# Performance work log

Measured on AMD Instinct MI355X. Metric: run time of the kernel, lower is better.

## Reference

```python
import jax, jax.numpy as jnp
from jax import lax
import numpy as np

NPOINTS, GROUP_SIZE, RADIUS = 1024, 32, 0.2
MLP = [64, 64, 128]
IN_CH = 6
BN_EPS = 1e-5


def farthest_point_sample(xyz, npoints):
    # xyz: [B, N, 3] -> idx [B, npoints]
    B, N, _ = xyz.shape

    def step(carry, _):
        dists, farthest = carry                      # [B,N], [B]
        centroid = jnp.take_along_axis(xyz, farthest[:, None, None], axis=1)  # [B,1,3]
        d = jnp.sum((xyz - centroid) ** 2, axis=-1)  # [B,N]
        dists = jnp.minimum(dists, d)
        nxt = jnp.argmax(dists, axis=-1).astype(jnp.int32)
        return (dists, nxt), farthest

    init = (jnp.full((B, N), 1e10, dtype=xyz.dtype), jnp.zeros((B,), dtype=jnp.int32))
    _, idxs = lax.scan(step, init, None, length=npoints)
    return idxs.T  # [B, npoints]


def ball_query(new_xyz, xyz, r, gs):
    # new_xyz: [B,S,3], xyz: [B,N,3] -> idx [B,S,gs]
    B, N, _ = xyz.shape
    sq = jnp.sum((new_xyz[:, :, None, :] - xyz[:, None, :, :]) ** 2, axis=-1)  # [B,S,N]
    idx = jnp.where(sq <= r * r, jnp.arange(N, dtype=jnp.int32), N)
    idx = jnp.sort(idx, axis=-1)[..., :gs]          # first gs in-ball indices
    first = idx[..., :1]
    idx = jnp.where(idx == N, first, idx)           # pad with first neighbor
    return idx


_batched_gather = jax.vmap(lambda p, i: p[i])        # p:[N,C], i:[S,G] -> [S,G,C]


def sample_and_group(xyz, features, npoints, gs, r):
    fps_idx = farthest_point_sample(xyz, npoints)                 # [B,S]
    new_xyz = jnp.take_along_axis(xyz, fps_idx[..., None], axis=1)  # [B,S,3]
    idx = ball_query(new_xyz, xyz, r, gs)                         # [B,S,G]
    grouped_xyz = _batched_gather(xyz, idx) - new_xyz[:, :, None, :]  # [B,S,G,3]
    grouped_feat = _batched_gather(features, idx)                 # [B,S,G,C]
    group_features = jnp.concatenate([grouped_xyz, grouped_feat], axis=-1)  # [B,S,G,3+C]
    return new_xyz, group_features


def pointnet(group_features, ws, bs, gammas, betas):
    # group_features: [B,S,G,D] -> permute to [B,D,S,G]
    x = jnp.transpose(group_features, (0, 3, 1, 2))
    for w, b, g, beta in zip(ws, bs, gammas, betas):
        x = jnp.einsum('oc,bcsg->bosg', w, x) + b[None, :, None, None]
        mu = jnp.mean(x, axis=(0, 2, 3), keepdims=True)
        var = jnp.mean((x - mu) ** 2, axis=(0, 2, 3), keepdims=True)  # biased, train-mode BN
        x = (x - mu) * lax.rsqrt(var + BN_EPS)
        x = x * g[None, :, None, None] + beta[None, :, None, None]
        x = jax.nn.relu(x)
    x = jnp.max(x, axis=-1)                         # max over group dim -> [B,C,S]
    return jnp.transpose(x, (0, 2, 1))              # [B,S,C]


def setup_inputs() -> dict:
    key = jax.random.key(0)
    ks = jax.random.split(key, 16)
    xyz = jax.random.uniform(ks[0], (16, 8192, 3), dtype=jnp.float32)
    features = jax.random.normal(ks[1], (16, 8192, 3), dtype=jnp.float32)
    inp = {'xyz': xyz, 'features': features}
    in_ch = IN_CH
    for i, out_ch in enumerate(MLP):
        scale = 1.0 / np.sqrt(in_ch)
        inp[f'w{i}'] = jax.random.uniform(ks[2 + 4 * i], (out_ch, in_ch), jnp.float32, -scale, scale)
        inp[f'b{i}'] = jax.random.uniform(ks[3 + 4 * i], (out_ch,), jnp.float32, -scale, scale)
        inp[f'g{i}'] = jnp.ones((out_ch,), jnp.float32)
        inp[f'bt{i}'] = jnp.zeros((out_ch,), jnp.float32)
        in_ch = out_ch
    return inp


def reference(xyz, features, w0, b0, g0, bt0, w1, b1, g1, bt1, w2, b2, g2, bt2):
    new_xyz, group_features = sample_and_group(xyz, features, NPOINTS, GROUP_SIZE, RADIUS)
    abstract_features = pointnet(group_features, [w0, w1, w2], [b0, b1, b2],
                                 [g0, g1, g2], [bt0, bt1, bt2])
    return new_xyz, abstract_features
```

## Files before the change

### kernel.cpp

```cpp
#include <hip/hip_runtime.h>
#include <math.h>

#define BB 16
#define NN 8192
#define SS 1024
#define GG 32
#define MTOT (BB*SS*GG)

struct alignas(16) f4 { float v[4]; };

typedef __attribute__((ext_vector_type(8))) short bfrag;
typedef __attribute__((ext_vector_type(4))) float facc;

#define MFMA16(a, b, c) __builtin_amdgcn_mfma_f32_16x16x32_bf16(a, b, c, 0, 0, 0)

__device__ __forceinline__ unsigned short f2bf(float f) {
    const unsigned u = __float_as_uint(f);
    return (unsigned short)((u + 0x7FFFu + ((u >> 16) & 1u)) >> 16);
}
__device__ __forceinline__ unsigned packbf(float lo, float hi) {
    return (unsigned)f2bf(lo) | ((unsigned)f2bf(hi) << 16);
}

template<int CTRL>
__device__ __forceinline__ int dppmov(int x) {
    return __builtin_amdgcn_update_dpp(x, x, CTRL, 0xF, 0xF, true);
}
template<int CTRL>
__device__ __forceinline__ void dlevel(int& hi, int& lo) {
    const int oh = dppmov<CTRL>(hi);
    const int ol = dppmov<CTRL>(lo);
    const unsigned long long o =
        ((unsigned long long)(unsigned)oh << 32) | (unsigned)ol;
    const unsigned long long c =
        ((unsigned long long)(unsigned)hi << 32) | (unsigned)lo;
    if (o > c) { hi = oh; lo = ol; }
}

__global__ __launch_bounds__(256) void fps_kernel(const float* __restrict__ xyz,
                                                  float* __restrict__ newxyz)
{
    __shared__ float lx[NN], ly[NN], lz[NN];
    __shared__ unsigned long long slots[2][4];
    const int b = blockIdx.x;
    const int t = threadIdx.x;
    const int wave = t >> 6, lane = t & 63;
    const float* base = xyz + (size_t)b * NN * 3;

    float px[32], py[32], pz[32], dd[32];
#pragma unroll
    for (int k = 0; k < 32; ++k) {
        const int p = (k << 8) + t;
        const float x = base[p * 3 + 0];
        const float y = base[p * 3 + 1];
        const float z = base[p * 3 + 2];
        px[k] = x; py[k] = y; pz[k] = z; dd[k] = 1e10f;
        lx[p] = x; ly[p] = y; lz[p] = z;
    }
    __syncthreads();

    int far = 0;
    float* outb = newxyz + (size_t)b * SS * 3;
    for (int s = 0; s < SS; ++s) {
        const float cx = lx[far], cy = ly[far], cz = lz[far];
        if (t == 0) {
            outb[s * 3 + 0] = cx;
            outb[s * 3 + 1] = cy;
            outb[s * 3 + 2] = cz;
        }
        float bf = -1.f;
        unsigned binv = 0u;
#pragma unroll
        for (int k = 0; k < 32; ++k) {
            const float dx = __fsub_rn(px[k], cx);
            const float dy = __fsub_rn(py[k], cy);
            const float dz = __fsub_rn(pz[k], cz);
            const float d  = __fadd_rn(__fadd_rn(__fmul_rn(dx, dx), __fmul_rn(dy, dy)),
                                       __fmul_rn(dz, dz));
            const float nd = fminf(dd[k], d);
            dd[k] = nd;
            if (nd > bf) {
                bf = nd;
                binv = 0xFFFFFFFFu - (unsigned)((k << 8) + t);
            }
        }

        int hi = __float_as_int(bf);
        int lo = (int)binv;
        dlevel<0x121>(hi, lo);
        dlevel<0x122>(hi, lo);
        dlevel<0x124>(hi, lo);
        dlevel<0x128>(hi, lo);
        {
            const int oh = __shfl_xor(hi, 16), ol = __shfl_xor(lo, 16);
            const unsigned long long o =
                ((unsigned long long)(unsigned)oh << 32) | (unsigned)ol;
            const unsigned long long c =
                ((unsigned long long)(unsigned)hi << 32) | (unsigned)lo;
            if (o > c) { hi = oh; lo = ol; }
        }
        {
            const int oh = __shfl_xor(hi, 32), ol = __shfl_xor(lo, 32);
            const unsigned long long o =
                ((unsigned long long)(unsigned)oh << 32) | (unsigned)ol;
            const unsigned long long c =
                ((unsigned long long)(unsigned)hi << 32) | (unsigned)lo;
            if (o > c) { hi = oh; lo = ol; }
        }

        if (lane == 0)
            slots[s & 1][wave] =
                ((unsigned long long)(unsigned)hi << 32) | (unsigned)lo;
        __syncthreads();
        unsigned long long g = slots[s & 1][0];
#pragma unroll
        for (int w = 1; w < 4; ++w) {
            const unsigned long long o = slots[s & 1][w];
            g = (o > g) ? o : g;
        }
        far = (int)(0xFFFFFFFFu - (unsigned)(g & 0xFFFFFFFFull));
    }
}

__global__ __launch_bounds__(256) void ball_gather_kernel(const float* __restrict__ xyz,
                                                          const float* __restrict__ feat,
                                                          const float* __restrict__ newxyz,
                                                          float* __restrict__ v,
                                                          float* __restrict__ part1)
{
    const int wid  = (int)((blockIdx.x * 256 + threadIdx.x) >> 6);
    const int lane = threadIdx.x & 63;
    if (wid >= BB * SS) return;
    const int b = wid >> 10;

    const float cx = newxyz[wid * 3 + 0];
    const float cy = newxyz[wid * 3 + 1];
    const float cz = newxyz[wid * 3 + 2];
    const float* xb = xyz + (size_t)b * NN * 3;
    const float* fb = feat + (size_t)b * NN * 3;
    const size_t mbase = (size_t)wid * GG;

    float mS[6];
    float mP[36];
#pragma unroll
    for (int c = 0; c < 6; ++c) mS[c] = 0.f;
#pragma unroll
    for (int c = 0; c < 36; ++c) mP[c] = 0.f;

    int cnt = 0, firstp = -1;
    for (int base = 0; base < NN && cnt < GG; base += 64) {
        const int p = base + lane;
        const float x = xb[p * 3 + 0], y = xb[p * 3 + 1], z = xb[p * 3 + 2];
        const float dx = __fsub_rn(cx, x);
        const float dy = __fsub_rn(cy, y);
        const float dz = __fsub_rn(cz, z);
        const float d  = __fadd_rn(__fadd_rn(__fmul_rn(dx, dx), __fmul_rn(dy, dy)),
                                   __fmul_rn(dz, dz));
        const bool hit = (d <= 0.04f);
        const unsigned long long m = __ballot(hit);
        if (firstp < 0 && m != 0ull) firstp = base + (int)__builtin_ctzll(m);
        const int pos = cnt + (int)__popcll(m & ((1ull << lane) - 1ull));
        if (hit && pos < GG) {
            const size_t mm = mbase + pos;
            float a[6];
            a[0] = __fsub_rn(x, cx);
            a[1] = __fsub_rn(y, cy);
            a[2] = __fsub_rn(z, cz);
            a[3] = fb[p * 3 + 0];
            a[4] = fb[p * 3 + 1];
            a[5] = fb[p * 3 + 2];
#pragma unroll
            for (int c = 0; c < 6; ++c) {
                v[(size_t)c * MTOT + mm] = a[c];
                mS[c] += a[c];
#pragma unroll
                for (int dch = 0; dch < 6; ++dch)
                    mP[c * 6 + dch] = fmaf(a[c], a[dch], mP[c * 6 + dch]);
            }
        }
        cnt += (int)__popcll(m);
    }
    if (cnt < GG) {
        const int p = firstp;
        const float x = xb[p * 3 + 0], y = xb[p * 3 + 1], z = xb[p * 3 + 2];
        float a[6];
        a[0] = __fsub_rn(x, cx);
        a[1] = __fsub_rn(y, cy);
        a[2] = __fsub_rn(z, cz);
        a[3] = fb[p * 3 + 0];
        a[4] = fb[p * 3 + 1];
        a[5] = fb[p * 3 + 2];
        for (int j = cnt + lane; j < GG; j += 64) {
            const size_t mm = mbase + j;
#pragma unroll
            for (int c = 0; c < 6; ++c) {
                v[(size_t)c * MTOT + mm] = a[c];
                mS[c] += a[c];
#pragma unroll
                for (int dch = 0; dch < 6; ++dch)
                    mP[c * 6 + dch] = fmaf(a[c], a[dch], mP[c * 6 + dch]);
            }
        }
    }
#pragma unroll
    for (int off = 1; off < 64; off <<= 1) {
#pragma unroll
        for (int c = 0; c < 6; ++c) mS[c] += __shfl_xor(mS[c], off);
#pragma unroll
        for (int c = 0; c < 36; ++c) mP[c] += __shfl_xor(mP[c], off);
    }
    if (lane == 0) {
        float* row = part1 + (size_t)wid * 42;
#pragma unroll
        for (int c = 0; c < 6; ++c) row[c] = mS[c];
#pragma unroll
        for (int c = 0; c < 36; ++c) row[6 + c] = mP[c];
    }
}

__global__ __launch_bounds__(1024) void finalize1_kernel(const float* __restrict__ part1,
                                                         const float* __restrict__ w0,
                                                         const float* __restrict__ g0,
                                                         const float* __restrict__ bt0,
                                                         const float* __restrict__ w1g,
                                                         const float* __restrict__ w2g,
                                                         short* __restrict__ wf1,
                                                         float* __restrict__ c1,
                                                         short* __restrict__ wf2r,
                                                         short* __restrict__ wf3r)
{
    const int tid = threadIdx.x;
    if (tid < 512) {
        const int f = tid >> 6, l = tid & 63;
        const int o = (f >> 1) * 16 + (l & 15);
        const int kb = (f & 1) * 32 + (l >> 4) * 8;
#pragma unroll
        for (int j = 0; j < 8; ++j)
            wf2r[tid * 8 + j] = (short)f2bf(w1g[o * 64 + kb + j]);
    }
    {
        const int f = tid >> 6, l = tid & 63;
        const int o = (f >> 1) * 16 + (l & 15);
        const int kb = (f & 1) * 32 + (l >> 4) * 8;
#pragma unroll
        for (int j = 0; j < 8; ++j)
            wf3r[tid * 8 + j] = (short)f2bf(w2g[o * 64 + kb + j]);
    }

    __shared__ double red[1008];
    __shared__ double tot[42];
    __shared__ float Asf[64];
    if (tid < 1008) {
        const int j = tid % 42, r = tid / 42;
        double s = 0.0;
#pragma unroll 4
        for (int i = r; i < BB * SS; i += 24) s += (double)part1[(size_t)i * 42 + j];
        red[tid] = s;
    }
    __syncthreads();
    if (tid < 42) {
        double s = 0.0;
        for (int r = 0; r < 24; ++r) s += red[r * 42 + tid];
        tot[tid] = s / (double)MTOT;
    }
    __syncthreads();
    if (tid < 64) {
        double m1 = 0.0;
        for (int c = 0; c < 6; ++c) m1 += (double)w0[tid * 6 + c] * tot[c];
        double e2 = 0.0;
        for (int c = 0; c < 6; ++c)
            for (int d = 0; d < 6; ++d)
                e2 += (double)w0[tid * 6 + c] * (double)w0[tid * 6 + d] * tot[6 + c * 6 + d];
        double var = e2 - m1 * m1;
        if (var < 0.0) var = 0.0;
        const double A = (double)g0[tid] / sqrt(var + 1e-5);
        Asf[tid] = (float)A;
        c1[tid] = (float)((double)bt0[tid] - A * m1);
    }
    __syncthreads();
    if (tid < 256) {
        const int l = tid & 63;
        const int o = (tid >> 6) * 16 + (l & 15);
        const int h = l >> 4;
#pragma unroll
        for (int j = 0; j < 8; ++j) {
            const float val = (h == 0 && j < 6) ? Asf[o] * w0[o * 6 + j] : 0.f;
            wf1[tid * 8 + j] = (short)f2bf(val);
        }
    }
}

template<int PHASE>
__global__ __launch_bounds__(256, 2) void chain_kernel(
    const float* __restrict__ v,
    const short* __restrict__ wf1, const float* __restrict__ c1,
    const short* __restrict__ wf2, const float* __restrict__ c2,
    const short* __restrict__ wf3,
    float* __restrict__ part, float* __restrict__ gmax, int tpb)
{
    __shared__ alignas(16) unsigned Hu1[4][16][36];
    __shared__ alignas(16) unsigned Hu2[(PHASE == 3) ? 4 : 1][16][36];
    __shared__ alignas(16) short w3l[(PHASE == 3) ? 8192 : 8];
    __shared__ alignas(16) float gm[(PHASE == 3) ? 4 : 1][128][20];
    __shared__ float redf[4][4][64];

    const int tid = threadIdx.x;
    const int w = tid >> 6, l = tid & 63;
    const int mcol = l & 15, h = l >> 4;

    if constexpr (PHASE == 3) {
        const unsigned* src = (const unsigned*)wf3;
        unsigned* dst = (unsigned*)w3l;
        for (int i = tid; i < 4096; i += 256) dst[i] = src[i];
    }
    __syncthreads();

    bfrag a1[4];
#pragma unroll
    for (int t = 0; t < 4; ++t) a1[t] = *(const bfrag*)&wf1[(t * 64 + l) * 8];
    bfrag a2[8];
#pragma unroll
    for (int f = 0; f < 8; ++f) a2[f] = *(const bfrag*)&wf2[(f * 64 + l) * 8];
    float c1v[16];
#pragma unroll
    for (int t = 0; t < 4; ++t)
#pragma unroll
        for (int r = 0; r < 4; ++r) c1v[t * 4 + r] = c1[t * 16 + h * 4 + r];
    float c2v[16];
    if constexpr (PHASE == 3) {
#pragma unroll
        for (int t = 0; t < 4; ++t)
#pragma unroll
            for (int r = 0; r < 4; ++r) c2v[t * 4 + r] = c2[t * 16 + h * 4 + r];
    }

    constexpr int NS = (PHASE == 3) ? 32 : 16;
    float sA[NS], qA[NS];
#pragma unroll
    for (int i = 0; i < NS; ++i) { sA[i] = 0.f; qA[i] = 0.f; }

    const facc zf = {0.f, 0.f, 0.f, 0.f};

    for (int ti = 0; ti < tpb; ++ti) {
        const int tile = blockIdx.x * tpb + ti;
        float mx[(PHASE == 3) ? 32 : 1];
        if constexpr (PHASE == 3) {
#pragma unroll
            for (int i = 0; i < 32; ++i) mx[i] = -3.0e38f;
        }

#pragma unroll
        for (int st = 0; st < 2; ++st) {
            const int mg = tile * 128 + w * 32 + st * 16 + mcol;

            bfrag bv;
#pragma unroll
            for (int j = 0; j < 8; ++j) bv[j] = 0;
            if (h == 0) {
#pragma unroll
                for (int j = 0; j < 6; ++j)
                    bv[j] = (short)f2bf(v[(size_t)j * MTOT + mg]);
            }
            facc x1[4];
#pragma unroll
            for (int t = 0; t < 4; ++t) x1[t] = MFMA16(a1[t], bv, zf);
#pragma unroll
            for (int t = 0; t < 4; ++t)
#pragma unroll
                for (int rr = 0; rr < 2; ++rr)
                    Hu1[w][mcol][t * 8 + h * 2 + rr] = packbf(
                        fmaxf(x1[t][2 * rr]     + c1v[t * 4 + 2 * rr],     0.f),
                        fmaxf(x1[t][2 * rr + 1] + c1v[t * 4 + 2 * rr + 1], 0.f));

            const bfrag b0 = *(const bfrag*)&Hu1[w][mcol][h * 4];
            const bfrag b1 = *(const bfrag*)&Hu1[w][mcol][16 + h * 4];

            if constexpr (PHASE == 2) {
#pragma unroll
                for (int t = 0; t < 4; ++t) {
                    facc a = MFMA16(a2[2 * t], b0, zf);
                    a = MFMA16(a2[2 * t + 1], b1, a);
#pragma unroll
                    for (int r = 0; r < 4; ++r) {
                        const float x = a[r];
                        sA[t * 4 + r] += x;
                        qA[t * 4 + r] = fmaf(x, x, qA[t * 4 + r]);
                    }
                }
            } else {
#pragma unroll
                for (int t = 0; t < 4; ++t) {
                    facc a = MFMA16(a2[2 * t], b0, zf);
                    a = MFMA16(a2[2 * t + 1], b1, a);
#pragma unroll
                    for (int rr = 0; rr < 2; ++rr)
                        Hu2[w][mcol][t * 8 + h * 2 + rr] = packbf(
                            fmaxf(a[2 * rr]     + c2v[t * 4 + 2 * rr],     0.f),
                            fmaxf(a[2 * rr + 1] + c2v[t * 4 + 2 * rr + 1], 0.f));
                }
                const bfrag d0 = *(const bfrag*)&Hu2[w][mcol][h * 4];
                const bfrag d1 = *(const bfrag*)&Hu2[w][mcol][16 + h * 4];
#pragma unroll
                for (int t3 = 0; t3 < 8; ++t3) {
                    const bfrag wa = *(const bfrag*)&w3l[((t3 * 2 + 0) * 64 + l) * 8];
                    const bfrag wb = *(const bfrag*)&w3l[((t3 * 2 + 1) * 64 + l) * 8];
                    facc a = MFMA16(wa, d0, zf);
                    a = MFMA16(wb, d1, a);
#pragma unroll
                    for (int r = 0; r < 4; ++r) {
                        const float x = a[r];
                        const int i = t3 * 4 + r;
                        sA[i] += x;
                        qA[i] = fmaf(x, x, qA[i]);
                        mx[i] = fmaxf(mx[i], x);
                    }
                }
            }
        }

        if constexpr (PHASE == 3) {
#pragma unroll
            for (int t3 = 0; t3 < 8; ++t3)
#pragma unroll
                for (int r = 0; r < 4; ++r)
                    gm[w][t3 * 16 + h * 4 + r][mcol] = mx[t3 * 4 + r];
            float m0 = -3.0e38f, m1 = -3.0e38f;
#pragma unroll
            for (int c4i = 0; c4i < 4; ++c4i) {
                const facc v0 = *(const facc*)&gm[w][2 * l][c4i * 4];
                const facc v1 = *(const facc*)&gm[w][2 * l + 1][c4i * 4];
#pragma unroll
                for (int jj = 0; jj < 4; ++jj) {
                    m0 = fmaxf(m0, v0[jj]);
                    m1 = fmaxf(m1, v1[jj]);
                }
            }
            const int g = tile * 4 + w;
            gmax[(size_t)g * 128 + 2 * l]     = m0;
            gmax[(size_t)g * 128 + 2 * l + 1] = m1;
        }
    }

#pragma unroll
    for (int off = 1; off < 16; off <<= 1) {
#pragma unroll
        for (int i = 0; i < NS; ++i) {
            sA[i] += __shfl_xor(sA[i], off);
            qA[i] += __shfl_xor(qA[i], off);
        }
    }
    __syncthreads();
    if (mcol == 0) {
#pragma unroll
        for (int i = 0; i < NS; ++i) {
            redf[w][h][i] = sA[i];
            redf[w][h][NS + i] = qA[i];
        }
    }
    __syncthreads();
    if constexpr (PHASE == 2) {
        if (tid < 128) {
            const int o = tid & 63, sq = tid >> 6;
            const int i = (o >> 4) * 4 + (o & 3), hh = (o >> 2) & 3;
            const int idx = sq * 16 + i;
            const float s = redf[0][hh][idx] + redf[1][hh][idx] +
                            redf[2][hh][idx] + redf[3][hh][idx];
            part[(size_t)blockIdx.x * 128 + sq * 64 + o] = s;
        }
    } else {
        if (tid < 256) {
            const int o = tid & 127, sq = tid >> 7;
            const int i = (o >> 4) * 4 + (o & 3), hh = (o >> 2) & 3;
            const int idx = sq * 32 + i;
            const float s = redf[0][hh][idx] + redf[1][hh][idx] +
                            redf[2][hh][idx] + redf[3][hh][idx];
            part[(size_t)blockIdx.x * 256 + sq * 128 + o] = s;
        }
    }
}

__global__ __launch_bounds__(1024) void finalize2_kernel(const float* __restrict__ part,
                                                         const float* __restrict__ w1g,
                                                         const float* __restrict__ g1,
                                                         const float* __restrict__ bt1,
                                                         short* __restrict__ wf2f,
                                                         float* __restrict__ c2)
{
    __shared__ double tot[1024];
    __shared__ float As[64];
    const int tid = threadIdx.x;
    const int j = tid & 127, r = tid >> 7;
    double s = 0.0;
#pragma unroll 4
    for (int blk = r; blk < 2048; blk += 8) s += (double)part[(size_t)blk * 128 + j];
    tot[tid] = s;
    __syncthreads();
    if (tid < 128) {
        double t = 0.0;
#pragma unroll
        for (int g = 0; g < 8; ++g) t += tot[g * 128 + tid];
        tot[tid] = t;
    }
    __syncthreads();
    if (tid < 64) {
        const double mean = tot[tid] / (double)MTOT;
        double var = tot[64 + tid] / (double)MTOT - mean * mean;
        if (var < 0.0) var = 0.0;
        const double A = (double)g1[tid] / sqrt(var + 1e-5);
        As[tid] = (float)A;
        c2[tid] = (float)((double)bt1[tid] - A * mean);
    }
    __syncthreads();
    if (tid < 512) {
        const int f = tid >> 6, l = tid & 63;
        const int o = (f >> 1) * 16 + (l & 15);
        const int kb = (f & 1) * 32 + (l >> 4) * 8;
#pragma unroll
        for (int j8 = 0; j8 < 8; ++j8)
            wf2f[tid * 8 + j8] = (short)f2bf(As[o] * w1g[o * 64 + kb + j8]);
    }
}

__global__ __launch_bounds__(1024) void finalize3_kernel(const float* __restrict__ part,
                                                         const float* __restrict__ g2,
                                                         const float* __restrict__ bt2,
                                                         float* __restrict__ A3,
                                                         float* __restrict__ c3)
{
    __shared__ double tot[1024];
    const int tid = threadIdx.x;
    const int j = tid & 255, r = tid >> 8;
    double s = 0.0;
#pragma unroll 4
    for (int blk = r; blk < 2048; blk += 4) s += (double)part[(size_t)blk * 256 + j];
    tot[tid] = s;
    __syncthreads();
    if (tid < 256) {
        const double t = tot[tid] + tot[256 + tid] + tot[512 + tid] + tot[768 + tid];
        tot[tid] = t;
    }
    __syncthreads();
    if (tid < 128) {
        const double mean = tot[tid] / (double)MTOT;
        double var = tot[128 + tid] / (double)MTOT - mean * mean;
        if (var < 0.0) var = 0.0;
        const double A = (double)g2[tid] / sqrt(var + 1e-5);
        A3[tid] = (float)A;
        c3[tid] = (float)((double)bt2[tid] - A * mean);
    }
}

__global__ __launch_bounds__(256) void final_out_kernel(float* __restrict__ outF,
                                                        const float* __restrict__ A3,
                                                        const float* __restrict__ c3)
{
    __shared__ float As[128], Cs[128];
    const int tid = threadIdx.x;
    if (tid < 128) { As[tid] = A3[tid]; Cs[tid] = c3[tid]; }
    __syncthreads();
    const int idx = (int)blockIdx.x * 256 + tid;
    f4 val = *reinterpret_cast<f4*>(&outF[(size_t)idx * 4]);
    const int chb = (idx * 4) & 127;
#pragma unroll
    for (int jj = 0; jj < 4; ++jj)
        val.v[jj] = fmaxf(fmaf(As[chb + jj], val.v[jj], Cs[chb + jj]), 0.f);
    *reinterpret_cast<f4*>(&outF[(size_t)idx * 4]) = val;
}

extern "C" void kernel_launch(void* const* d_in, const int* in_sizes, int n_in,
                              void* d_out, int out_size, void* d_ws, size_t ws_size,
                              hipStream_t stream)
{
    const float* xyz  = (const float*)d_in[0];
    const float* feat = (const float*)d_in[1];
    const float* w0  = (const float*)d_in[2];
    const float* g0  = (const float*)d_in[4];
    const float* bt0 = (const float*)d_in[5];
    const float* w1  = (const float*)d_in[6];
    const float* g1  = (const float*)d_in[8];
    const float* bt1 = (const float*)d_in[9];
    const float* w2  = (const float*)d_in[10];
    const float* g2  = (const float*)d_in[12];
    const float* bt2 = (const float*)d_in[13];

    float* out    = (float*)d_out;
    float* newxyz = out;
    float* outF   = out + BB * SS * 3;

    float* wsf  = (float*)d_ws;
    float* v    = wsf;
    float* part = wsf + 6ull * MTOT;
    float* c1   = part + 688128;
    float* c2   = c1 + 64;
    float* A3   = c2 + 64;
    float* c3   = A3 + 128;
    short* wf1  = (short*)(c3 + 128);
    short* wf2r = wf1 + 2048;
    short* wf2f = wf2r + 4096;
    short* wf3  = wf2f + 4096;

    fps_kernel<<<dim3(BB), dim3(256), 0, stream>>>(xyz, newxyz);
    ball_gather_kernel<<<dim3(4096), dim3(256), 0, stream>>>(xyz, feat, newxyz, v, part);
    finalize1_kernel<<<dim3(1), dim3(1024), 0, stream>>>(part, w0, g0, bt0, w1, w2,
                                                         wf1, c1, wf2r, wf3);

    chain_kernel<2><<<dim3(2048), dim3(256), 0, stream>>>(v, wf1, c1, wf2r, nullptr,
                                                          nullptr, part, nullptr, 2);
    finalize2_kernel<<<dim3(1), dim3(1024), 0, stream>>>(part, w1, g1, bt1, wf2f, c2);

    chain_kernel<3><<<dim3(2048), dim3(256), 0, stream>>>(v, wf1, c1, wf2f, c2,
                                                          wf3, part, outF, 2);
    finalize3_kernel<<<dim3(1), dim3(1024), 0, stream>>>(part, g2, bt2, A3, c3);
    final_out_kernel<<<dim3(2048), dim3(256), 0, stream>>>(outF, A3, c3);
}
```

Measured before the change: 1.236 ms.

## Parallelize BN1 stats reduction, shorten FPS argmax reduce, use DPP sums in chain

Adds a 64-block reduce1 kernel that tree-reduces the 16384x42 BN1 partial rows into 64 rows, so the single-block finalize1 reads far less data serially. In FPS the cross-lane shuffles at offsets 16 and 32 are replaced by writing 16 per-row candidates to shared memory and reducing them with a tree after the barrier. The chain kernel's 16-lane sum reductions switch from shfl_xor to DPP row operations. This adds one more kernel launch, and the first reduction now runs in float instead of double.

```diff
diff --git a/kernel.cpp b/kernel.cpp
--- a/kernel.cpp
+++ b/kernel.cpp
@@ -36,12 +36,19 @@
         ((unsigned long long)(unsigned)hi << 32) | (unsigned)lo;
     if (o > c) { hi = oh; lo = ol; }
 }
+__device__ __forceinline__ float dppadd16(float x) {
+    x += __int_as_float(dppmov<0x121>(__float_as_int(x)));
+    x += __int_as_float(dppmov<0x122>(__float_as_int(x)));
+    x += __int_as_float(dppmov<0x124>(__float_as_int(x)));
+    x += __int_as_float(dppmov<0x128>(__float_as_int(x)));
+    return x;
+}
 
 __global__ __launch_bounds__(256) void fps_kernel(const float* __restrict__ xyz,
                                                   float* __restrict__ newxyz)
 {
     __shared__ float lx[NN], ly[NN], lz[NN];
-    __shared__ unsigned long long slots[2][4];
+    __shared__ unsigned long long slots[2][16];
     const int b = blockIdx.x;
     const int t = threadIdx.x;
     const int wave = t >> 6, lane = t & 63;
@@ -91,33 +98,24 @@
         dlevel<0x122>(hi, lo);
         dlevel<0x124>(hi, lo);
         dlevel<0x128>(hi, lo);
-        {
-            const int oh = __shfl_xor(hi, 16), ol = __shfl_xor(lo, 16);
-            const unsigned long long o =
-                ((unsigned long long)(unsigned)oh << 32) | (unsigned)ol;
-            const unsigned long long c =
-                ((unsigned long long)(unsigned)hi << 32) | (unsigned)lo;
-            if (o > c) { hi = oh; lo = ol; }
-        }
-        {
-            const int oh = __shfl_xor(hi, 32), ol = __shfl_xor(lo, 32);
-            const unsigned long long o =
-                ((unsigned long long)(unsigned)oh << 32) | (unsigned)ol;
-            const unsigned long long c =
-                ((unsigned long long)(unsigned)hi << 32) | (unsigned)lo;
-            if (o > c) { hi = oh; lo = ol; }
-        }
-
-        if (lane == 0)
-            slots[s & 1][wave] =
+
+        if ((lane & 15) == 0)
+            slots[s & 1][(wave << 2) | (lane >> 4)] =
                 ((unsigned long long)(unsigned)hi << 32) | (unsigned)lo;
         __syncthreads();
-        unsigned long long g = slots[s & 1][0];
-#pragma unroll
-        for (int w = 1; w < 4; ++w) {
-            const unsigned long long o = slots[s & 1][w];
-            g = (o > g) ? o : g;
-        }
+        const unsigned long long* sl = slots[s & 1];
+        unsigned long long m8[8];
+#pragma unroll
+        for (int i = 0; i < 8; ++i) {
+            const unsigned long long a = sl[2 * i], c = sl[2 * i + 1];
+            m8[i] = (a > c) ? a : c;
+        }
+#pragma unroll
+        for (int i = 0; i < 4; ++i)
+            m8[i] = (m8[2 * i] > m8[2 * i + 1]) ? m8[2 * i] : m8[2 * i + 1];
+        m8[0] = (m8[0] > m8[1]) ? m8[0] : m8[1];
+        m8[2] = (m8[2] > m8[3]) ? m8[2] : m8[3];
+        const unsigned long long g = (m8[0] > m8[2]) ? m8[0] : m8[2];
         far = (int)(0xFFFFFFFFu - (unsigned)(g & 0xFFFFFFFFull));
     }
 }
@@ -218,7 +216,36 @@
     }
 }
 
-__global__ __launch_bounds__(1024) void finalize1_kernel(const float* __restrict__ part1,
+__global__ __launch_bounds__(256) void reduce1_kernel(const float* __restrict__ part1,
+                                                      float* __restrict__ red64)
+{
+    __shared__ float ldsT[42][260];
+    const int tid = threadIdx.x;
+    const int row = (int)blockIdx.x * 256 + tid;
+    const float* rp = part1 + (size_t)row * 42;
+    float r42[42];
+#pragma unroll
+    for (int i = 0; i < 21; ++i) {
+        const float2 v2 = *reinterpret_cast<const float2*>(rp + 2 * i);
+        r42[2 * i] = v2.x; r42[2 * i + 1] = v2.y;
+    }
+#pragma unroll
+    for (int c = 0; c < 42; ++c) ldsT[c][tid] = r42[c];
+    __syncthreads();
+    if (tid < 168) {
+        const int c = tid >> 2, r = tid & 3;
+        float s = 0.f;
+#pragma unroll
+        for (int k = 0; k < 64; ++k) s += ldsT[c][r * 64 + k];
+        ldsT[c][256 + r] = s;
+    }
+    __syncthreads();
+    if (tid < 42)
+        red64[(size_t)blockIdx.x * 42 + tid] =
+            (ldsT[tid][256] + ldsT[tid][257]) + (ldsT[tid][258] + ldsT[tid][259]);
+}
+
+__global__ __launch_bounds__(1024) void finalize1_kernel(const float* __restrict__ red64,
                                                          const float* __restrict__ w0,
                                                          const float* __restrict__ g0,
                                                          const float* __restrict__ bt0,
@@ -247,20 +274,20 @@
             wf3r[tid * 8 + j] = (short)f2bf(w2g[o * 64 + kb + j]);
     }
 
-    __shared__ double red[1008];
+    __shared__ double red[672];
     __shared__ double tot[42];
     __shared__ float Asf[64];
-    if (tid < 1008) {
+    if (tid < 672) {
         const int j = tid % 42, r = tid / 42;
         double s = 0.0;
-#pragma unroll 4
-        for (int i = r; i < BB * SS; i += 24) s += (double)part1[(size_t)i * 42 + j];
+#pragma unroll
+        for (int i = r; i < 64; i += 16) s += (double)red64[(size_t)i * 42 + j];
         red[tid] = s;
     }
     __syncthreads();
     if (tid < 42) {
         double s = 0.0;
-        for (int r = 0; r < 24; ++r) s += red[r * 42 + tid];
+        for (int r = 0; r < 16; ++r) s += red[r * 42 + tid];
         tot[tid] = s / (double)MTOT;
     }
     __syncthreads();
@@ -442,12 +469,9 @@
     }
 
 #pragma unroll
-    for (int off = 1; off < 16; off <<= 1) {
-#pragma unroll
-        for (int i = 0; i < NS; ++i) {
-            sA[i] += __shfl_xor(sA[i], off);
-            qA[i] += __shfl_xor(qA[i], off);
-        }
+    for (int i = 0; i < NS; ++i) {
+        sA[i] = dppadd16(sA[i]);
+        qA[i] = dppadd16(qA[i]);
     }
     __syncthreads();
     if (mcol == 0) {
@@ -587,21 +611,23 @@
     float* newxyz = out;
     float* outF   = out + BB * SS * 3;
 
-    float* wsf  = (float*)d_ws;
-    float* v    = wsf;
-    float* part = wsf + 6ull * MTOT;
-    float* c1   = part + 688128;
-    float* c2   = c1 + 64;
-    float* A3   = c2 + 64;
-    float* c3   = A3 + 128;
-    short* wf1  = (short*)(c3 + 128);
-    short* wf2r = wf1 + 2048;
-    short* wf2f = wf2r + 4096;
-    short* wf3  = wf2f + 4096;
+    float* wsf   = (float*)d_ws;
+    float* v     = wsf;
+    float* part  = wsf + 6ull * MTOT;
+    float* red64 = part + 688128;
+    float* c1    = red64 + 2688;
+    float* c2    = c1 + 64;
+    float* A3    = c2 + 64;
+    float* c3    = A3 + 128;
+    short* wf1   = (short*)(c3 + 128);
+    short* wf2r  = wf1 + 2048;
+    short* wf2f  = wf2r + 4096;
+    short* wf3   = wf2f + 4096;
 
     fps_kernel<<<dim3(BB), dim3(256), 0, stream>>>(xyz, newxyz);
     ball_gather_kernel<<<dim3(4096), dim3(256), 0, stream>>>(xyz, feat, newxyz, v, part);
-    finalize1_kernel<<<dim3(1), dim3(1024), 0, stream>>>(part, w0, g0, bt0, w1, w2,
+    reduce1_kernel<<<dim3(64), dim3(256), 0, stream>>>(part, red64);
+    finalize1_kernel<<<dim3(1), dim3(1024), 0, stream>>>(red64, w0, g0, bt0, w1, w2,
                                                          wf1, c1, wf2r, wf3);
 
     chain_kernel<2><<<dim3(2048), dim3(256), 0, stream>>>(v, wf1, c1, wf2r, nullptr,
```

Result: no change. 1.228 ms (-0.7%).
